# Kernel tuning notes

Hardware: AMD Instinct MI355X
Metric: run time of the kernel (lower is better)

Reference implementation:

```python
import jax, jax.numpy as jnp
import numpy as np
from jax import lax

GLOBAL_BITS = 5
N_LEVELS = float(2 ** GLOBAL_BITS - 1)  # 31


@jax.custom_vjp
def sigmoid_quant(x):
    # round(x * n * 0.4) / n, clamped to [0, 1]
    return jnp.clip(jnp.round(x * (N_LEVELS * 0.4)) / N_LEVELS, 0.0, 1.0)

def _sigq_fwd(x):
    return sigmoid_quant(x), x

def _sigq_bwd(x, g):
    # STE: pass-through, zeroed where |x| >= 2.5 (torch uses ge/le)
    return (jnp.where((x >= 2.5) | (x <= -2.5), 0.0, g),)

sigmoid_quant.defvjp(_sigq_fwd, _sigq_bwd)


@jax.custom_vjp
def tanh_quant(x):
    # round(x * n) / n, clamped to [-1, 1]
    return jnp.clip(jnp.round(x * N_LEVELS) / N_LEVELS, -1.0, 1.0)

def _tanhq_fwd(x):
    return tanh_quant(x), x

def _tanhq_bwd(x, g):
    return (jnp.where((x >= 1.0) | (x <= -1.0), 0.0, g),)

tanh_quant.defvjp(_tanhq_fwd, _tanhq_bwd)


def gru_layer(x, Wh, bh, Wz, bz, Wr, br, Uh, Uz, Ur):
    """x: [T, B, D_in] -> hiddens [T, B, H]. Quantized GRU, test mode (drop=0)."""
    T, B, _ = x.shape
    H = Wh.shape[0]
    # Precompute input projections over all timesteps (as the torch code does).
    wh = jnp.einsum('tbd,hd->tbh', x, Wh) + bh
    wz = jnp.einsum('tbd,hd->tbh', x, Wz) + bz
    wr = jnp.einsum('tbd,hd->tbh', x, Wr) + br

    def step(h, gates):
        whk, wzk, wrk = gates
        zt = sigmoid_quant(wzk + h @ Uz.T)
        rt = sigmoid_quant(wrk + h @ Ur.T)
        at = whk + (rt * h) @ Uh.T
        hcand = tanh_quant(at)  # drop_mask == 1.0 in test mode
        h_new = zt * h + (1.0 - zt) * hcand
        return h_new, h_new

    h0 = jnp.zeros((B, H), dtype=x.dtype)
    _, hs = lax.scan(step, h0, (wh, wz, wr))
    return hs


def _layer_params(key, d_in, h):
    ks = jax.random.split(key, 6)
    s_in = 1.0 / np.sqrt(d_in)
    s_h = 1.0 / np.sqrt(h)
    return dict(
        Wh=jax.random.uniform(ks[0], (h, d_in), jnp.float32, -s_in, s_in),
        bh=jnp.zeros((h,), jnp.float32),
        Wz=jax.random.uniform(ks[1], (h, d_in), jnp.float32, -s_in, s_in),
        bz=jnp.zeros((h,), jnp.float32),
        Wr=jax.random.uniform(ks[2], (h, d_in), jnp.float32, -s_in, s_in),
        br=jnp.zeros((h,), jnp.float32),
        Uh=jax.random.uniform(ks[3], (h, h), jnp.float32, -s_h, s_h),
        Uz=jax.random.uniform(ks[4], (h, h), jnp.float32, -s_h, s_h),
        Ur=jax.random.uniform(ks[5], (h, h), jnp.float32, -s_h, s_h),
    )


def setup_inputs() -> dict:
    T, B, D, H, C = 200, 512, 40, 400, 12
    key = jax.random.key(0)
    kx, k0, k1, kfc = jax.random.split(key, 4)
    inp = {"x": jax.random.normal(kx, (T, B, D), jnp.float32)}
    p0 = _layer_params(k0, D, H)
    p1 = _layer_params(k1, H, H)
    for name, v in p0.items():
        inp[name + "0"] = v
    for name, v in p1.items():
        inp[name + "1"] = v
    s = 1.0 / np.sqrt(H)
    inp["Wfc"] = jax.random.uniform(kfc, (C, H), jnp.float32, -s, s)
    inp["bfc"] = jnp.zeros((C,), jnp.float32)
    return inp


def reference(x, Wh0, bh0, Wz0, bz0, Wr0, br0, Uh0, Uz0, Ur0,
              Wh1, bh1, Wz1, bz1, Wr1, br1, Uh1, Uz1, Ur1, Wfc, bfc):
    h = gru_layer(x, Wh0, bh0, Wz0, bz0, Wr0, br0, Uh0, Uz0, Ur0)
    h = gru_layer(h, Wh1, bh1, Wz1, bz1, Wr1, br1, Uh1, Uz1, Ur1)
    out = h[-1]                 # [B, H] last timestep
    logits = out @ Wfc.T + bfc  # [B, C]
    return jax.nn.softmax(logits, axis=-1)
```

## Files before the change

### kernel.cpp

```cpp
#include <hip/hip_runtime.h>
#include <math.h>

#define TT 200
#define BB 512
#define DD 40
#define HH 400
#define NC 12
#define NBLK 500
#define NTHR 256


struct P {
  const float *x;
  const float *Wh0,*bh0,*Wz0,*bz0,*Wr0,*br0,*Uh0,*Uz0,*Ur0;
  const float *Wh1,*bh1,*Wz1,*bz1,*Wr1,*br1,*Uh1,*Uz1,*Ur1;
  const float *Wfc,*bfc;
  float *h0a,*h0b,*h1a,*h1b;
  float *rt1,*zt1,*ah1p,*rt0n,*zt0n;
  unsigned *bar;
  float *out;
};

__device__ __forceinline__ float sigq(float x){
  float v = rintf(x * 12.4f) / 31.0f;
  return fminf(fmaxf(v, 0.0f), 1.0f);
}
__device__ __forceinline__ float tanhq(float x){
  float v = rintf(x * 31.0f) / 31.0f;
  return fminf(fmaxf(v, -1.0f), 1.0f);
}

__device__ void load_slice(float* dst, const float* __restrict__ Wg, int ldw,
                           int j0, int K, int tid){
  const int c  = tid >> 4;
  const int ks = tid & 15;
  for (int k = ks; k < K; k += 16)
    dst[k*16 + c] = Wg[(size_t)(j0 + c)*ldw + k];
}

__device__ __forceinline__ void gaccL(const float* __restrict__ A, int lda,
                                      const float* __restrict__ Wl,
                                      int r, int cb, int K, float acc[2][4]){
  const float4* a0 = (const float4*)(A + (size_t)r*lda);
  const float4* a1 = (const float4*)(A + (size_t)r*lda + lda);
  const int K4 = K >> 2;
  #pragma unroll 4
  for (int k = 0; k < K4; ++k) {
    float4 av0 = a0[k], av1 = a1[k];
    float a0v[4] = {av0.x, av0.y, av0.z, av0.w};
    float a1v[4] = {av1.x, av1.y, av1.z, av1.w};
    #pragma unroll
    for (int i = 0; i < 4; ++i) {
      float4 wv = *(const float4*)(Wl + (k*4+i)*16 + cb);
      acc[0][0]+=a0v[i]*wv.x; acc[0][1]+=a0v[i]*wv.y; acc[0][2]+=a0v[i]*wv.z; acc[0][3]+=a0v[i]*wv.w;
      acc[1][0]+=a1v[i]*wv.x; acc[1][1]+=a1v[i]*wv.y; acc[1][2]+=a1v[i]*wv.z; acc[1][3]+=a1v[i]*wv.w;
    }
  }
}

__device__ __forceinline__ void paccL(const float* __restrict__ Ap,
                                      const float* __restrict__ Am,
                                      const float* __restrict__ Wl,
                                      int r, int cb, int K, float acc[2][4]){
  const float4* p0 = (const float4*)(Ap + (size_t)r*HH);
  const float4* p1 = (const float4*)(Ap + (size_t)r*HH + HH);
  const float4* m0 = (const float4*)(Am + (size_t)r*HH);
  const float4* m1 = (const float4*)(Am + (size_t)r*HH + HH);
  const int K4 = K >> 2;
  #pragma unroll 4
  for (int k = 0; k < K4; ++k) {
    float4 pv0 = p0[k], mv0 = m0[k], pv1 = p1[k], mv1 = m1[k];
    float a0v[4] = {pv0.x*mv0.x, pv0.y*mv0.y, pv0.z*mv0.z, pv0.w*mv0.w};
    float a1v[4] = {pv1.x*mv1.x, pv1.y*mv1.y, pv1.z*mv1.z, pv1.w*mv1.w};
    #pragma unroll
    for (int i = 0; i < 4; ++i) {
      float4 wv = *(const float4*)(Wl + (k*4+i)*16 + cb);
      acc[0][0]+=a0v[i]*wv.x; acc[0][1]+=a0v[i]*wv.y; acc[0][2]+=a0v[i]*wv.z; acc[0][3]+=a0v[i]*wv.w;
      acc[1][0]+=a1v[i]*wv.x; acc[1][1]+=a1v[i]*wv.y; acc[1][2]+=a1v[i]*wv.z; acc[1][3]+=a1v[i]*wv.w;
    }
  }
}

__device__ __forceinline__ void gaccG(const float* __restrict__ A, int lda,
                                      const float* __restrict__ W, int ldw,
                                      int r, int c0, int K, float acc[2][4]){
  const float4* a0 = (const float4*)(A + (size_t)r*lda);
  const float4* a1 = (const float4*)(A + (size_t)r*lda + lda);
  const int K4 = K >> 2;
  for (int k = 0; k < K4; ++k) {
    float4 av0 = a0[k], av1 = a1[k];
    #pragma unroll
    for (int j = 0; j < 4; ++j) {
      float4 wv = *(const float4*)(W + (size_t)(c0+j)*ldw + k*4);
      acc[0][j]+=av0.x*wv.x; acc[0][j]+=av0.y*wv.y; acc[0][j]+=av0.z*wv.z; acc[0][j]+=av0.w*wv.w;
      acc[1][j]+=av1.x*wv.x; acc[1][j]+=av1.y*wv.y; acc[1][j]+=av1.z*wv.z; acc[1][j]+=av1.w*wv.w;
    }
  }
}

__device__ void beta_wave(const P& p, int t, int bm, int bj0, int r, int cb,
                          const float* Wb0, const float* Wb1){
  const float* h0n = (t & 1) ? p.h0b : p.h0a;
  const float* h1c = (t & 1) ? p.h1b : p.h1a;
  const float* xt1 = p.x + (size_t)((t+1) % TT) * BB * DD;
  float acc[2][4] = {};
  const float* bias; float* out; int act = 1;
  if (bm == 0)      { gaccL(h1c,HH,Wb0,r,cb,HH,acc); gaccL(h0n,HH,Wb1,r,cb,HH,acc); bias=p.br1; out=p.rt1; }
  else if (bm == 1) { gaccL(h1c,HH,Wb0,r,cb,HH,acc); gaccL(h0n,HH,Wb1,r,cb,HH,acc); bias=p.bz1; out=p.zt1; }
  else if (bm == 2) { gaccL(h0n,HH,Wb0,r,cb,HH,acc); bias=p.bh1; out=p.ah1p; act=0; }
  else if (bm == 3) { gaccL(h0n,HH,Wb0,r,cb,HH,acc); gaccL(xt1,DD,Wb1,r,cb,DD,acc); bias=p.br0; out=p.rt0n; }
  else              { gaccL(h0n,HH,Wb0,r,cb,HH,acc); gaccL(xt1,DD,Wb1,r,cb,DD,acc); bias=p.bz0; out=p.zt0n; }
  const int c0 = bj0 + cb;
  #pragma unroll
  for (int i = 0; i < 2; ++i) {
    float4 v;
    v.x = acc[i][0] + bias[c0+0];
    v.y = acc[i][1] + bias[c0+1];
    v.z = acc[i][2] + bias[c0+2];
    v.w = acc[i][3] + bias[c0+3];
    if (act) { v.x = sigq(v.x); v.y = sigq(v.y); v.z = sigq(v.z); v.w = sigq(v.w); }
    *(float4*)(out + (size_t)(r+i)*HH + c0) = v;
  }
}

__device__ void alpha_wave(const P& p, int t, int am, int aj0, int r, int cb,
                           const float* Wa, const float* Wa2){
  const float* h0n = (t & 1) ? p.h0b : p.h0a;
  const float* h1c = (t & 1) ? p.h1b : p.h1a;
  float* h0w = (t & 1) ? p.h0a : p.h0b;
  float* h1w = (t & 1) ? p.h1a : p.h1b;
  const float* xt1 = p.x + (size_t)((t+1) % TT) * BB * DD;
  float acc[2][4] = {};
  const int c0 = aj0 + cb;
  if (am == 0) {
    paccL(p.rt1, h1c, Wa, r, cb, HH, acc);
    #pragma unroll
    for (int i = 0; i < 2; ++i) {
      size_t base = (size_t)(r+i)*HH + c0;
      float4 ap = *(const float4*)(p.ah1p + base);
      float4 z  = *(const float4*)(p.zt1 + base);
      float4 hv = *(const float4*)(h1c + base);
      float4 o;
      o.x = z.x*hv.x + (1.0f - z.x)*tanhq(acc[i][0] + ap.x);
      o.y = z.y*hv.y + (1.0f - z.y)*tanhq(acc[i][1] + ap.y);
      o.z = z.z*hv.z + (1.0f - z.z)*tanhq(acc[i][2] + ap.z);
      o.w = z.w*hv.w + (1.0f - z.w)*tanhq(acc[i][3] + ap.w);
      *(float4*)(h1w + base) = o;
    }
  } else {
    paccL(p.rt0n, h0n, Wa, r, cb, HH, acc);
    gaccL(xt1, DD, Wa2, r, cb, DD, acc);
    #pragma unroll
    for (int i = 0; i < 2; ++i) {
      size_t base = (size_t)(r+i)*HH + c0;
      float4 z  = *(const float4*)(p.zt0n + base);
      float4 hv = *(const float4*)(h0n + base);
      float4 o;
      o.x = z.x*hv.x + (1.0f - z.x)*tanhq(acc[i][0] + p.bh0[c0+0]);
      o.y = z.y*hv.y + (1.0f - z.y)*tanhq(acc[i][1] + p.bh0[c0+1]);
      o.z = z.z*hv.z + (1.0f - z.z)*tanhq(acc[i][2] + p.bh0[c0+2]);
      o.w = z.w*hv.w + (1.0f - z.w)*tanhq(acc[i][3] + p.bh0[c0+3]);
      *(float4*)(h0w + base) = o;
    }
  }
}

__device__ void pro_wave(const P& p, int coltile, int r, int cb){
  const int c0 = coltile*16 + cb;
  float accz[2][4] = {}, acca[2][4] = {};
  gaccG(p.x, DD, p.Wz0, DD, r, c0, DD, accz);
  gaccG(p.x, DD, p.Wh0, DD, r, c0, DD, acca);
  #pragma unroll
  for (int i = 0; i < 2; ++i) {
    float4 o;
    float z;
    z = sigq(accz[i][0] + p.bz0[c0+0]); o.x = (1.0f - z)*tanhq(acca[i][0] + p.bh0[c0+0]);
    z = sigq(accz[i][1] + p.bz0[c0+1]); o.y = (1.0f - z)*tanhq(acca[i][1] + p.bh0[c0+1]);
    z = sigq(accz[i][2] + p.bz0[c0+2]); o.z = (1.0f - z)*tanhq(acca[i][2] + p.bh0[c0+2]);
    z = sigq(accz[i][3] + p.bz0[c0+3]); o.w = (1.0f - z)*tanhq(acca[i][3] + p.bh0[c0+3]);
    *(float4*)(p.h0a + (size_t)(r+i)*HH + c0) = o;
  }
}

__device__ void fc_wave(const P& p, int b, int lane){
  const float* h1 = p.h1a;
  float l[NC];
  #pragma unroll
  for (int cI = 0; cI < NC; ++cI) {
    float sm = 0.0f;
    for (int k = lane; k < HH; k += 64)
      sm += h1[(size_t)b*HH + k] * p.Wfc[(size_t)cI*HH + k];
    #pragma unroll
    for (int off = 32; off > 0; off >>= 1)
      sm += __shfl_xor(sm, off);
    l[cI] = sm + p.bfc[cI];
  }
  float mx = l[0];
  #pragma unroll
  for (int cI = 1; cI < NC; ++cI) mx = fmaxf(mx, l[cI]);
  float sum = 0.0f;
  #pragma unroll
  for (int cI = 0; cI < NC; ++cI) { l[cI] = expf(l[cI] - mx); sum += l[cI]; }
  float inv = 1.0f / sum;
  if (lane == 0) {
    #pragma unroll
    for (int cI = 0; cI < NC; ++cI) p.out[(size_t)b*NC + cI] = l[cI] * inv;
  }
}

__device__ void gbar(int bn, unsigned* bar, int u){
  __syncthreads();
  if (threadIdx.x == 0) {
    __threadfence();
    const int i = u & 15;
    const int quota = (NBLK >> 4) + ((i < (NBLK & 15)) ? 1 : 0);
    unsigned* c0  = bar + i*32;
    unsigned* c1  = bar + 512;
    unsigned* gen = bar + 544;
    unsigned v = __hip_atomic_fetch_add(c0, 1u, __ATOMIC_RELEASE, __HIP_MEMORY_SCOPE_AGENT);
    if (v + 1u == (unsigned)quota * (unsigned)(bn+1)) {
      unsigned w2 = __hip_atomic_fetch_add(c1, 1u, __ATOMIC_ACQ_REL, __HIP_MEMORY_SCOPE_AGENT);
      if (w2 + 1u == 16u * (unsigned)(bn+1))
        __hip_atomic_store(gen, (unsigned)(bn+1), __ATOMIC_RELEASE, __HIP_MEMORY_SCOPE_AGENT);
    }
    while (__hip_atomic_load(gen, __ATOMIC_RELAXED, __HIP_MEMORY_SCOPE_AGENT) < (unsigned)(bn+1))
      __builtin_amdgcn_s_sleep(2);
    __threadfence();
  }
  __syncthreads();
}

__device__ void load_beta_lds(const P& p, int bm, int bj0, float* Wb0, float* Wb1, int tid){
  if (bm == 0)      { load_slice(Wb0, p.Ur1, HH, bj0, HH, tid); load_slice(Wb1, p.Wr1, HH, bj0, HH, tid); }
  else if (bm == 1) { load_slice(Wb0, p.Uz1, HH, bj0, HH, tid); load_slice(Wb1, p.Wz1, HH, bj0, HH, tid); }
  else if (bm == 2) { load_slice(Wb0, p.Wh1, HH, bj0, HH, tid); }
  else if (bm == 3) { load_slice(Wb0, p.Ur0, HH, bj0, HH, tid); load_slice(Wb1, p.Wr0, DD, bj0, DD, tid); }
  else              { load_slice(Wb0, p.Uz0, HH, bj0, HH, tid); load_slice(Wb1, p.Wz0, DD, bj0, DD, tid); }
}
__device__ void load_alpha_lds(const P& p, int am, int aj0, float* Wa, float* Wa2, int tid){
  if (am == 0) load_slice(Wa, p.Uh1, HH, aj0, HH, tid);
  else       { load_slice(Wa, p.Uh0, HH, aj0, HH, tid); load_slice(Wa2, p.Wh0, DD, aj0, DD, tid); }
}

__global__ __launch_bounds__(NTHR, 2) void gru_coop(P p){
  __shared__ float lds[19840];
  float* Wb0 = lds;
  float* Wb1 = lds + 6400;
  float* Wa  = lds + 12800;
  float* Wa2 = lds + 19200;

  const int u    = blockIdx.x;
  const int tid  = threadIdx.x;
  const int w    = tid >> 6;
  const int lane = tid & 63;

  const int bkey = u >> 2, bq = u & 3;
  const int bm = bkey / 25, bj0 = (bkey % 25) * 16;
  const int akey = u >> 2;
  const int am = akey / 25, aj0 = (akey % 25) * 16;

  const int r  = bq*128 + w*32 + (lane & 15)*2;
  const int cb = (lane >> 4) * 4;

  load_beta_lds(p, bm, bj0, Wb0, Wb1, tid);
  if (u < 200) load_alpha_lds(p, am, aj0, Wa, Wa2, tid);
  if (u < 100) pro_wave(p, u >> 2, (u & 3)*128 + w*32 + (lane & 15)*2, cb);

  int bn = 0;
  gbar(bn++, p.bar, u);
  for (int t = 0; t < TT; ++t) {
    beta_wave(p, t, bm, bj0, r, cb, Wb0, Wb1);
    gbar(bn++, p.bar, u);
    if (u < 200) alpha_wave(p, t, am, aj0, r, cb, Wa, Wa2);
    gbar(bn++, p.bar, u);
  }
  if (u < 128) fc_wave(p, u*4 + w, lane);
}

__global__ __launch_bounds__(NTHR) void k_pro(P p){
  const int u = blockIdx.x, tid = threadIdx.x, w = tid >> 6, lane = tid & 63;
  pro_wave(p, u >> 2, (u & 3)*128 + w*32 + (lane & 15)*2, ((lane >> 4)*4));
}
__global__ __launch_bounds__(NTHR) void k_beta(P p, int t){
  __shared__ float lds[12800];
  const int u = blockIdx.x, tid = threadIdx.x, w = tid >> 6, lane = tid & 63;
  const int bkey = u >> 2, bq = u & 3;
  const int bm = bkey / 25, bj0 = (bkey % 25) * 16;
  load_beta_lds(p, bm, bj0, lds, lds + 6400, tid);
  __syncthreads();
  beta_wave(p, t, bm, bj0, bq*128 + w*32 + (lane & 15)*2, (lane >> 4)*4, lds, lds + 6400);
}
__global__ __launch_bounds__(NTHR) void k_alpha(P p, int t){
  __shared__ float lds[7040];
  const int u = blockIdx.x, tid = threadIdx.x, w = tid >> 6, lane = tid & 63;
  const int akey = u >> 2, aq = u & 3;
  const int am = akey / 25, aj0 = (akey % 25) * 16;
  load_alpha_lds(p, am, aj0, lds, lds + 6400, tid);
  __syncthreads();
  alpha_wave(p, t, am, aj0, aq*128 + w*32 + (lane & 15)*2, (lane >> 4)*4, lds, lds + 6400);
}
__global__ __launch_bounds__(NTHR) void k_fc(P p){
  const int w = threadIdx.x >> 6, lane = threadIdx.x & 63;
  fc_wave(p, blockIdx.x*4 + w, lane);
}

extern "C" void kernel_launch(void* const* d_in, const int* in_sizes, int n_in,
                              void* d_out, int out_size, void* d_ws, size_t ws_size,
                              hipStream_t stream) {
  P p;
  p.x   = (const float*)d_in[0];
  p.Wh0 = (const float*)d_in[1];  p.bh0 = (const float*)d_in[2];
  p.Wz0 = (const float*)d_in[3];  p.bz0 = (const float*)d_in[4];
  p.Wr0 = (const float*)d_in[5];  p.br0 = (const float*)d_in[6];
  p.Uh0 = (const float*)d_in[7];  p.Uz0 = (const float*)d_in[8];  p.Ur0 = (const float*)d_in[9];
  p.Wh1 = (const float*)d_in[10]; p.bh1 = (const float*)d_in[11];
  p.Wz1 = (const float*)d_in[12]; p.bz1 = (const float*)d_in[13];
  p.Wr1 = (const float*)d_in[14]; p.br1 = (const float*)d_in[15];
  p.Uh1 = (const float*)d_in[16]; p.Uz1 = (const float*)d_in[17]; p.Ur1 = (const float*)d_in[18];
  p.Wfc = (const float*)d_in[19]; p.bfc = (const float*)d_in[20];

  float* ws = (float*)d_ws;
  const size_t SZ = (size_t)BB * HH;
  p.h0a  = ws + 0*SZ;  p.h0b  = ws + 1*SZ;
  p.h1a  = ws + 2*SZ;  p.h1b  = ws + 3*SZ;
  p.rt1  = ws + 4*SZ;  p.zt1  = ws + 5*SZ;  p.ah1p = ws + 6*SZ;
  p.rt0n = ws + 7*SZ;  p.zt0n = ws + 8*SZ;
  p.bar  = (unsigned*)(ws + 9*SZ);
  p.out  = (float*)d_out;

  hipMemsetAsync(p.h1a, 0, SZ*sizeof(float), stream);
  hipMemsetAsync(p.bar, 0, 4096, stream);

  void* args[] = { &p };
  hipError_t err = hipLaunchCooperativeKernel((const void*)gru_coop, dim3(NBLK),
                                              dim3(NTHR), args, 0, stream);
  if (err != hipSuccess) {
    k_pro<<<dim3(100), dim3(NTHR), 0, stream>>>(p);
    for (int t = 0; t < TT; ++t) {
      k_beta <<<dim3(NBLK), dim3(NTHR), 0, stream>>>(p, t);
      k_alpha<<<dim3(200),  dim3(NTHR), 0, stream>>>(p, t);
    }
    k_fc<<<dim3(128), dim3(NTHR), 0, stream>>>(p);
  }
}
```

Baseline: 33.75 ms.

## Transpose hidden-state layout to column-major and give each thread 16 output columns

Hidden state and gate buffers now use a [H][B] layout. Each thread owns one batch row and computes 16 output columns, so the LDS weight reads become broadcasts and the activation loads are coalesced. The grid is halved to 250 blocks. The input x is transposed into double-buffered xta/xtb scratch by idle blocks during the alpha phase. The cost is one batch element per thread with scalar strided loads and 16 accumulators per thread, which means fewer, fatter waves.

```diff
diff --git a/kernel.cpp b/kernel.cpp
--- a/kernel.cpp
+++ b/kernel.cpp
@@ -6,7 +6,7 @@
 #define DD 40
 #define HH 400
 #define NC 12
-#define NBLK 500
+#define NBLK 250
 #define NTHR 256
 
 
@@ -17,6 +17,7 @@
   const float *Wfc,*bfc;
   float *h0a,*h0b,*h1a,*h1b;
   float *rt1,*zt1,*ah1p,*rt0n,*zt0n;
+  float *xta,*xtb;
   unsigned *bar;
   float *out;
 };
@@ -32,153 +33,133 @@
 
 __device__ void load_slice(float* dst, const float* __restrict__ Wg, int ldw,
                            int j0, int K, int tid){
-  const int c  = tid >> 4;
-  const int ks = tid & 15;
-  for (int k = ks; k < K; k += 16)
+  const int c  = tid & 15;
+  const int kb = tid >> 4;
+  for (int k = kb; k < K; k += 16)
     dst[k*16 + c] = Wg[(size_t)(j0 + c)*ldw + k];
 }
 
-__device__ __forceinline__ void gaccL(const float* __restrict__ A, int lda,
+__device__ __forceinline__ void gaccT(const float* __restrict__ A,
                                       const float* __restrict__ Wl,
-                                      int r, int cb, int K, float acc[2][4]){
-  const float4* a0 = (const float4*)(A + (size_t)r*lda);
-  const float4* a1 = (const float4*)(A + (size_t)r*lda + lda);
+                                      int b, int K, float acc[16]){
+  const float* ap = A + b;
   const int K4 = K >> 2;
-  #pragma unroll 4
-  for (int k = 0; k < K4; ++k) {
-    float4 av0 = a0[k], av1 = a1[k];
-    float a0v[4] = {av0.x, av0.y, av0.z, av0.w};
-    float a1v[4] = {av1.x, av1.y, av1.z, av1.w};
-    #pragma unroll
-    for (int i = 0; i < 4; ++i) {
-      float4 wv = *(const float4*)(Wl + (k*4+i)*16 + cb);
-      acc[0][0]+=a0v[i]*wv.x; acc[0][1]+=a0v[i]*wv.y; acc[0][2]+=a0v[i]*wv.z; acc[0][3]+=a0v[i]*wv.w;
-      acc[1][0]+=a1v[i]*wv.x; acc[1][1]+=a1v[i]*wv.y; acc[1][2]+=a1v[i]*wv.z; acc[1][3]+=a1v[i]*wv.w;
-    }
-  }
-}
-
-__device__ __forceinline__ void paccL(const float* __restrict__ Ap,
+  #pragma unroll 2
+  for (int g = 0; g < K4; ++g) {
+    float a[4];
+    #pragma unroll
+    for (int kk = 0; kk < 4; ++kk) a[kk] = ap[(size_t)(g*4+kk)*BB];
+    #pragma unroll
+    for (int kk = 0; kk < 4; ++kk) {
+      const float4* w = (const float4*)(Wl + (g*4+kk)*16);
+      float4 w0 = w[0], w1 = w[1], w2 = w[2], w3 = w[3];
+      float av = a[kk];
+      acc[0] +=av*w0.x; acc[1] +=av*w0.y; acc[2] +=av*w0.z; acc[3] +=av*w0.w;
+      acc[4] +=av*w1.x; acc[5] +=av*w1.y; acc[6] +=av*w1.z; acc[7] +=av*w1.w;
+      acc[8] +=av*w2.x; acc[9] +=av*w2.y; acc[10]+=av*w2.z; acc[11]+=av*w2.w;
+      acc[12]+=av*w3.x; acc[13]+=av*w3.y; acc[14]+=av*w3.z; acc[15]+=av*w3.w;
+    }
+  }
+}
+
+__device__ __forceinline__ void paccT(const float* __restrict__ Ap,
                                       const float* __restrict__ Am,
                                       const float* __restrict__ Wl,
-                                      int r, int cb, int K, float acc[2][4]){
-  const float4* p0 = (const float4*)(Ap + (size_t)r*HH);
-  const float4* p1 = (const float4*)(Ap + (size_t)r*HH + HH);
-  const float4* m0 = (const float4*)(Am + (size_t)r*HH);
-  const float4* m1 = (const float4*)(Am + (size_t)r*HH + HH);
+                                      int b, int K, float acc[16]){
+  const float* pp = Ap + b;
+  const float* mp = Am + b;
   const int K4 = K >> 2;
-  #pragma unroll 4
-  for (int k = 0; k < K4; ++k) {
-    float4 pv0 = p0[k], mv0 = m0[k], pv1 = p1[k], mv1 = m1[k];
-    float a0v[4] = {pv0.x*mv0.x, pv0.y*mv0.y, pv0.z*mv0.z, pv0.w*mv0.w};
-    float a1v[4] = {pv1.x*mv1.x, pv1.y*mv1.y, pv1.z*mv1.z, pv1.w*mv1.w};
-    #pragma unroll
-    for (int i = 0; i < 4; ++i) {
-      float4 wv = *(const float4*)(Wl + (k*4+i)*16 + cb);
-      acc[0][0]+=a0v[i]*wv.x; acc[0][1]+=a0v[i]*wv.y; acc[0][2]+=a0v[i]*wv.z; acc[0][3]+=a0v[i]*wv.w;
-      acc[1][0]+=a1v[i]*wv.x; acc[1][1]+=a1v[i]*wv.y; acc[1][2]+=a1v[i]*wv.z; acc[1][3]+=a1v[i]*wv.w;
-    }
-  }
-}
-
-__device__ __forceinline__ void gaccG(const float* __restrict__ A, int lda,
-                                      const float* __restrict__ W, int ldw,
-                                      int r, int c0, int K, float acc[2][4]){
-  const float4* a0 = (const float4*)(A + (size_t)r*lda);
-  const float4* a1 = (const float4*)(A + (size_t)r*lda + lda);
-  const int K4 = K >> 2;
-  for (int k = 0; k < K4; ++k) {
-    float4 av0 = a0[k], av1 = a1[k];
-    #pragma unroll
-    for (int j = 0; j < 4; ++j) {
-      float4 wv = *(const float4*)(W + (size_t)(c0+j)*ldw + k*4);
-      acc[0][j]+=av0.x*wv.x; acc[0][j]+=av0.y*wv.y; acc[0][j]+=av0.z*wv.z; acc[0][j]+=av0.w*wv.w;
-      acc[1][j]+=av1.x*wv.x; acc[1][j]+=av1.y*wv.y; acc[1][j]+=av1.z*wv.z; acc[1][j]+=av1.w*wv.w;
-    }
-  }
-}
-
-__device__ void beta_wave(const P& p, int t, int bm, int bj0, int r, int cb,
+  #pragma unroll 2
+  for (int g = 0; g < K4; ++g) {
+    float a[4];
+    #pragma unroll
+    for (int kk = 0; kk < 4; ++kk)
+      a[kk] = pp[(size_t)(g*4+kk)*BB] * mp[(size_t)(g*4+kk)*BB];
+    #pragma unroll
+    for (int kk = 0; kk < 4; ++kk) {
+      const float4* w = (const float4*)(Wl + (g*4+kk)*16);
+      float4 w0 = w[0], w1 = w[1], w2 = w[2], w3 = w[3];
+      float av = a[kk];
+      acc[0] +=av*w0.x; acc[1] +=av*w0.y; acc[2] +=av*w0.z; acc[3] +=av*w0.w;
+      acc[4] +=av*w1.x; acc[5] +=av*w1.y; acc[6] +=av*w1.z; acc[7] +=av*w1.w;
+      acc[8] +=av*w2.x; acc[9] +=av*w2.y; acc[10]+=av*w2.z; acc[11]+=av*w2.w;
+      acc[12]+=av*w3.x; acc[13]+=av*w3.y; acc[14]+=av*w3.z; acc[15]+=av*w3.w;
+    }
+  }
+}
+
+__device__ void xpose(const float* __restrict__ xsrc, float* dst, int d, int tid){
+  for (int b = tid; b < BB; b += NTHR)
+    dst[d*BB + b] = xsrc[(size_t)b*DD + d];
+}
+
+__device__ void beta_wave(const P& p, int t, int bm, int c0, int b,
                           const float* Wb0, const float* Wb1){
   const float* h0n = (t & 1) ? p.h0b : p.h0a;
   const float* h1c = (t & 1) ? p.h1b : p.h1a;
-  const float* xt1 = p.x + (size_t)((t+1) % TT) * BB * DD;
-  float acc[2][4] = {};
+  const float* xt1 = (t & 1) ? p.xta : p.xtb;
+
+  float acc[16] = {};
   const float* bias; float* out; int act = 1;
-  if (bm == 0)      { gaccL(h1c,HH,Wb0,r,cb,HH,acc); gaccL(h0n,HH,Wb1,r,cb,HH,acc); bias=p.br1; out=p.rt1; }
-  else if (bm == 1) { gaccL(h1c,HH,Wb0,r,cb,HH,acc); gaccL(h0n,HH,Wb1,r,cb,HH,acc); bias=p.bz1; out=p.zt1; }
-  else if (bm == 2) { gaccL(h0n,HH,Wb0,r,cb,HH,acc); bias=p.bh1; out=p.ah1p; act=0; }
-  else if (bm == 3) { gaccL(h0n,HH,Wb0,r,cb,HH,acc); gaccL(xt1,DD,Wb1,r,cb,DD,acc); bias=p.br0; out=p.rt0n; }
-  else              { gaccL(h0n,HH,Wb0,r,cb,HH,acc); gaccL(xt1,DD,Wb1,r,cb,DD,acc); bias=p.bz0; out=p.zt0n; }
-  const int c0 = bj0 + cb;
-  #pragma unroll
-  for (int i = 0; i < 2; ++i) {
-    float4 v;
-    v.x = acc[i][0] + bias[c0+0];
-    v.y = acc[i][1] + bias[c0+1];
-    v.z = acc[i][2] + bias[c0+2];
-    v.w = acc[i][3] + bias[c0+3];
-    if (act) { v.x = sigq(v.x); v.y = sigq(v.y); v.z = sigq(v.z); v.w = sigq(v.w); }
-    *(float4*)(out + (size_t)(r+i)*HH + c0) = v;
-  }
-}
-
-__device__ void alpha_wave(const P& p, int t, int am, int aj0, int r, int cb,
+  if (bm == 0)      { gaccT(h1c,Wb0,b,HH,acc); gaccT(h0n,Wb1,b,HH,acc); bias=p.br1; out=p.rt1; }
+  else if (bm == 1) { gaccT(h1c,Wb0,b,HH,acc); gaccT(h0n,Wb1,b,HH,acc); bias=p.bz1; out=p.zt1; }
+  else if (bm == 2) { gaccT(h0n,Wb0,b,HH,acc); bias=p.bh1; out=p.ah1p; act=0; }
+  else if (bm == 3) { gaccT(h0n,Wb0,b,HH,acc); gaccT(xt1,Wb1,b,DD,acc); bias=p.br0; out=p.rt0n; }
+  else              { gaccT(h0n,Wb0,b,HH,acc); gaccT(xt1,Wb1,b,DD,acc); bias=p.bz0; out=p.zt0n; }
+
+  #pragma unroll
+  for (int c = 0; c < 16; ++c) {
+    float v = acc[c] + bias[c0+c];
+    out[(size_t)(c0+c)*BB + b] = act ? sigq(v) : v;
+  }
+}
+
+__device__ void alpha_wave(const P& p, int t, int am, int c0, int b,
                            const float* Wa, const float* Wa2){
   const float* h0n = (t & 1) ? p.h0b : p.h0a;
   const float* h1c = (t & 1) ? p.h1b : p.h1a;
   float* h0w = (t & 1) ? p.h0a : p.h0b;
   float* h1w = (t & 1) ? p.h1a : p.h1b;
-  const float* xt1 = p.x + (size_t)((t+1) % TT) * BB * DD;
-  float acc[2][4] = {};
-  const int c0 = aj0 + cb;
+  const float* xt1 = (t & 1) ? p.xta : p.xtb;
+
+  float acc[16] = {};
   if (am == 0) {
-    paccL(p.rt1, h1c, Wa, r, cb, HH, acc);
-    #pragma unroll
-    for (int i = 0; i < 2; ++i) {
-      size_t base = (size_t)(r+i)*HH + c0;
-      float4 ap = *(const float4*)(p.ah1p + base);
-      float4 z  = *(const float4*)(p.zt1 + base);
-      float4 hv = *(const float4*)(h1c + base);
-      float4 o;
-      o.x = z.x*hv.x + (1.0f - z.x)*tanhq(acc[i][0] + ap.x);
-      o.y = z.y*hv.y + (1.0f - z.y)*tanhq(acc[i][1] + ap.y);
-      o.z = z.z*hv.z + (1.0f - z.z)*tanhq(acc[i][2] + ap.z);
-      o.w = z.w*hv.w + (1.0f - z.w)*tanhq(acc[i][3] + ap.w);
-      *(float4*)(h1w + base) = o;
+    paccT(p.rt1, h1c, Wa, b, HH, acc);
+    #pragma unroll
+    for (int c = 0; c < 16; ++c) {
+      size_t idx = (size_t)(c0+c)*BB + b;
+      float at = acc[c] + p.ah1p[idx];
+      float z = p.zt1[idx], hv = h1c[idx];
+      h1w[idx] = z*hv + (1.0f - z)*tanhq(at);
     }
   } else {
-    paccL(p.rt0n, h0n, Wa, r, cb, HH, acc);
-    gaccL(xt1, DD, Wa2, r, cb, DD, acc);
-    #pragma unroll
-    for (int i = 0; i < 2; ++i) {
-      size_t base = (size_t)(r+i)*HH + c0;
-      float4 z  = *(const float4*)(p.zt0n + base);
-      float4 hv = *(const float4*)(h0n + base);
-      float4 o;
-      o.x = z.x*hv.x + (1.0f - z.x)*tanhq(acc[i][0] + p.bh0[c0+0]);
-      o.y = z.y*hv.y + (1.0f - z.y)*tanhq(acc[i][1] + p.bh0[c0+1]);
-      o.z = z.z*hv.z + (1.0f - z.z)*tanhq(acc[i][2] + p.bh0[c0+2]);
-      o.w = z.w*hv.w + (1.0f - z.w)*tanhq(acc[i][3] + p.bh0[c0+3]);
-      *(float4*)(h0w + base) = o;
-    }
-  }
-}
-
-__device__ void pro_wave(const P& p, int coltile, int r, int cb){
-  const int c0 = coltile*16 + cb;
-  float accz[2][4] = {}, acca[2][4] = {};
-  gaccG(p.x, DD, p.Wz0, DD, r, c0, DD, accz);
-  gaccG(p.x, DD, p.Wh0, DD, r, c0, DD, acca);
-  #pragma unroll
-  for (int i = 0; i < 2; ++i) {
-    float4 o;
-    float z;
-    z = sigq(accz[i][0] + p.bz0[c0+0]); o.x = (1.0f - z)*tanhq(acca[i][0] + p.bh0[c0+0]);
-    z = sigq(accz[i][1] + p.bz0[c0+1]); o.y = (1.0f - z)*tanhq(acca[i][1] + p.bh0[c0+1]);
-    z = sigq(accz[i][2] + p.bz0[c0+2]); o.z = (1.0f - z)*tanhq(acca[i][2] + p.bh0[c0+2]);
-    z = sigq(accz[i][3] + p.bz0[c0+3]); o.w = (1.0f - z)*tanhq(acca[i][3] + p.bh0[c0+3]);
-    *(float4*)(p.h0a + (size_t)(r+i)*HH + c0) = o;
+    paccT(p.rt0n, h0n, Wa, b, HH, acc);
+    gaccT(xt1, Wa2, b, DD, acc);
+    #pragma unroll
+    for (int c = 0; c < 16; ++c) {
+      size_t idx = (size_t)(c0+c)*BB + b;
+      float at = acc[c] + p.bh0[c0+c];
+      float z = p.zt0n[idx], hv = h0n[idx];
+      h0w[idx] = z*hv + (1.0f - z)*tanhq(at);
+    }
+  }
+}
+
+__device__ void pro_wave(const P& p, int c0, int b){
+  float az[16] = {}, ah[16] = {};
+  for (int d = 0; d < DD; ++d) {
+    float av = p.xta[d*BB + b];
+    #pragma unroll
+    for (int c = 0; c < 16; ++c) {
+      az[c] += av * p.Wz0[(size_t)(c0+c)*DD + d];
+      ah[c] += av * p.Wh0[(size_t)(c0+c)*DD + d];
+    }
+  }
+  #pragma unroll
+  for (int c = 0; c < 16; ++c) {
+    float z = sigq(az[c] + p.bz0[c0+c]);
+    float a = ah[c] + p.bh0[c0+c];
+    p.h0a[(size_t)(c0+c)*BB + b] = (1.0f - z)*tanhq(a);
   }
 }
 
@@ -189,7 +170,7 @@
   for (int cI = 0; cI < NC; ++cI) {
     float sm = 0.0f;
     for (int k = lane; k < HH; k += 64)
-      sm += h1[(size_t)b*HH + k] * p.Wfc[(size_t)cI*HH + k];
+      sm += h1[(size_t)k*BB + b] * p.Wfc[(size_t)cI*HH + k];
     #pragma unroll
     for (int off = 32; off > 0; off >>= 1)
       sm += __shfl_xor(sm, off);
@@ -230,16 +211,16 @@
   __syncthreads();
 }
 
-__device__ void load_beta_lds(const P& p, int bm, int bj0, float* Wb0, float* Wb1, int tid){
-  if (bm == 0)      { load_slice(Wb0, p.Ur1, HH, bj0, HH, tid); load_slice(Wb1, p.Wr1, HH, bj0, HH, tid); }
-  else if (bm == 1) { load_slice(Wb0, p.Uz1, HH, bj0, HH, tid); load_slice(Wb1, p.Wz1, HH, bj0, HH, tid); }
-  else if (bm == 2) { load_slice(Wb0, p.Wh1, HH, bj0, HH, tid); }
-  else if (bm == 3) { load_slice(Wb0, p.Ur0, HH, bj0, HH, tid); load_slice(Wb1, p.Wr0, DD, bj0, DD, tid); }
-  else              { load_slice(Wb0, p.Uz0, HH, bj0, HH, tid); load_slice(Wb1, p.Wz0, DD, bj0, DD, tid); }
-}
-__device__ void load_alpha_lds(const P& p, int am, int aj0, float* Wa, float* Wa2, int tid){
-  if (am == 0) load_slice(Wa, p.Uh1, HH, aj0, HH, tid);
-  else       { load_slice(Wa, p.Uh0, HH, aj0, HH, tid); load_slice(Wa2, p.Wh0, DD, aj0, DD, tid); }
+__device__ void load_beta_lds(const P& p, int bm, int j0, float* Wb0, float* Wb1, int tid){
+  if (bm == 0)      { load_slice(Wb0, p.Ur1, HH, j0, HH, tid); load_slice(Wb1, p.Wr1, HH, j0, HH, tid); }
+  else if (bm == 1) { load_slice(Wb0, p.Uz1, HH, j0, HH, tid); load_slice(Wb1, p.Wz1, HH, j0, HH, tid); }
+  else if (bm == 2) { load_slice(Wb0, p.Wh1, HH, j0, HH, tid); }
+  else if (bm == 3) { load_slice(Wb0, p.Ur0, HH, j0, HH, tid); load_slice(Wb1, p.Wr0, DD, j0, DD, tid); }
+  else              { load_slice(Wb0, p.Uz0, HH, j0, HH, tid); load_slice(Wb1, p.Wz0, DD, j0, DD, tid); }
+}
+__device__ void load_alpha_lds(const P& p, int am, int j0, float* Wa, float* Wa2, int tid){
+  if (am == 0) load_slice(Wa, p.Uh1, HH, j0, HH, tid);
+  else       { load_slice(Wa, p.Uh0, HH, j0, HH, tid); load_slice(Wa2, p.Wh0, DD, j0, DD, tid); }
 }
 
 __global__ __launch_bounds__(NTHR, 2) void gru_coop(P p){
@@ -249,59 +230,65 @@
   float* Wa  = lds + 12800;
   float* Wa2 = lds + 19200;
 
-  const int u    = blockIdx.x;
-  const int tid  = threadIdx.x;
-  const int w    = tid >> 6;
-  const int lane = tid & 63;
-
-  const int bkey = u >> 2, bq = u & 3;
-  const int bm = bkey / 25, bj0 = (bkey % 25) * 16;
-  const int akey = u >> 2;
-  const int am = akey / 25, aj0 = (akey % 25) * 16;
-
-  const int r  = bq*128 + w*32 + (lane & 15)*2;
-  const int cb = (lane >> 4) * 4;
-
-  load_beta_lds(p, bm, bj0, Wb0, Wb1, tid);
-  if (u < 200) load_alpha_lds(p, am, aj0, Wa, Wa2, tid);
-  if (u < 100) pro_wave(p, u >> 2, (u & 3)*128 + w*32 + (lane & 15)*2, cb);
-
+  const int u   = blockIdx.x;
+  const int tid = threadIdx.x;
+  const int bk  = u >> 1;
+  const int bm  = bk / 25, bc0 = (bk % 25) * 16;
+  const int am  = bk / 25, ac0 = bc0;
+  const int b   = (u & 1)*256 + tid;
+
+  load_beta_lds(p, bm, bc0, Wb0, Wb1, tid);
+  if (u < 100) load_alpha_lds(p, am, ac0, Wa, Wa2, tid);
+
+  if (u < 40)       xpose(p.x,                       p.xta, u,      tid);
+  else if (u < 80)  xpose(p.x + (size_t)BB*DD,       p.xtb, u - 40, tid);
   int bn = 0;
   gbar(bn++, p.bar, u);
+  if (u < 50) pro_wave(p, (u >> 1)*16, b);
+  gbar(bn++, p.bar, u);
+
   for (int t = 0; t < TT; ++t) {
-    beta_wave(p, t, bm, bj0, r, cb, Wb0, Wb1);
+    beta_wave(p, t, bm, bc0, b, Wb0, Wb1);
     gbar(bn++, p.bar, u);
-    if (u < 200) alpha_wave(p, t, am, aj0, r, cb, Wa, Wa2);
+    if (u < 100) alpha_wave(p, t, am, ac0, b, Wa, Wa2);
+    else if (u < 140)
+      xpose(p.x + (size_t)((t+2) % TT)*BB*DD, (t & 1) ? p.xtb : p.xta, u - 100, tid);
     gbar(bn++, p.bar, u);
   }
-  if (u < 128) fc_wave(p, u*4 + w, lane);
-}
-
+  if (u < 128) fc_wave(p, u*4 + (tid >> 6), tid & 63);
+}
+
+__global__ __launch_bounds__(NTHR) void k_init(P p){
+  const int u = blockIdx.x, tid = threadIdx.x;
+  if (u < 40)      xpose(p.x,                 p.xta, u,      tid);
+  else if (u < 80) xpose(p.x + (size_t)BB*DD, p.xtb, u - 40, tid);
+}
 __global__ __launch_bounds__(NTHR) void k_pro(P p){
-  const int u = blockIdx.x, tid = threadIdx.x, w = tid >> 6, lane = tid & 63;
-  pro_wave(p, u >> 2, (u & 3)*128 + w*32 + (lane & 15)*2, ((lane >> 4)*4));
+  const int u = blockIdx.x;
+  pro_wave(p, (u >> 1)*16, (u & 1)*256 + threadIdx.x);
 }
 __global__ __launch_bounds__(NTHR) void k_beta(P p, int t){
   __shared__ float lds[12800];
-  const int u = blockIdx.x, tid = threadIdx.x, w = tid >> 6, lane = tid & 63;
-  const int bkey = u >> 2, bq = u & 3;
-  const int bm = bkey / 25, bj0 = (bkey % 25) * 16;
-  load_beta_lds(p, bm, bj0, lds, lds + 6400, tid);
+  const int u = blockIdx.x, tid = threadIdx.x;
+  const int bk = u >> 1, bm = bk / 25, bc0 = (bk % 25) * 16;
+  load_beta_lds(p, bm, bc0, lds, lds + 6400, tid);
   __syncthreads();
-  beta_wave(p, t, bm, bj0, bq*128 + w*32 + (lane & 15)*2, (lane >> 4)*4, lds, lds + 6400);
+  beta_wave(p, t, bm, bc0, (u & 1)*256 + tid, lds, lds + 6400);
 }
 __global__ __launch_bounds__(NTHR) void k_alpha(P p, int t){
   __shared__ float lds[7040];
-  const int u = blockIdx.x, tid = threadIdx.x, w = tid >> 6, lane = tid & 63;
-  const int akey = u >> 2, aq = u & 3;
-  const int am = akey / 25, aj0 = (akey % 25) * 16;
-  load_alpha_lds(p, am, aj0, lds, lds + 6400, tid);
-  __syncthreads();
-  alpha_wave(p, t, am, aj0, aq*128 + w*32 + (lane & 15)*2, (lane >> 4)*4, lds, lds + 6400);
+  const int u = blockIdx.x, tid = threadIdx.x;
+  if (u < 100) {
+    const int ak = u >> 1, am = ak / 25, ac0 = (ak % 25) * 16;
+    load_alpha_lds(p, am, ac0, lds, lds + 6400, tid);
+    __syncthreads();
+    alpha_wave(p, t, am, ac0, (u & 1)*256 + tid, lds, lds + 6400);
+  } else if (u < 140) {
+    xpose(p.x + (size_t)((t+2) % TT)*BB*DD, (t & 1) ? p.xtb : p.xta, u - 100, tid);
+  }
 }
 __global__ __launch_bounds__(NTHR) void k_fc(P p){
-  const int w = threadIdx.x >> 6, lane = threadIdx.x & 63;
-  fc_wave(p, blockIdx.x*4 + w, lane);
+  fc_wave(p, blockIdx.x*4 + (threadIdx.x >> 6), threadIdx.x & 63);
 }
 
 extern "C" void kernel_launch(void* const* d_in, const int* in_sizes, int n_in,
@@ -325,7 +312,9 @@
   p.h1a  = ws + 2*SZ;  p.h1b  = ws + 3*SZ;
   p.rt1  = ws + 4*SZ;  p.zt1  = ws + 5*SZ;  p.ah1p = ws + 6*SZ;
   p.rt0n = ws + 7*SZ;  p.zt0n = ws + 8*SZ;
-  p.bar  = (unsigned*)(ws + 9*SZ);
+  p.xta  = ws + 9*SZ;
+  p.xtb  = p.xta + (size_t)BB*DD;
+  p.bar  = (unsigned*)(p.xtb + (size_t)BB*DD);
   p.out  = (float*)d_out;
 
   hipMemsetAsync(p.h1a, 0, SZ*sizeof(float), stream);
@@ -335,10 +324,11 @@
   hipError_t err = hipLaunchCooperativeKernel((const void*)gru_coop, dim3(NBLK),
                                               dim3(NTHR), args, 0, stream);
   if (err != hipSuccess) {
-    k_pro<<<dim3(100), dim3(NTHR), 0, stream>>>(p);
+    k_init<<<dim3(80), dim3(NTHR), 0, stream>>>(p);
+    k_pro<<<dim3(50), dim3(NTHR), 0, stream>>>(p);
     for (int t = 0; t < TT; ++t) {
       k_beta <<<dim3(NBLK), dim3(NTHR), 0, stream>>>(p, t);
-      k_alpha<<<dim3(200),  dim3(NTHR), 0, stream>>>(p, t);
+      k_alpha<<<dim3(140),  dim3(NTHR), 0, stream>>>(p, t);
     }
     k_fc<<<dim3(128), dim3(NTHR), 0, stream>>>(p);
   }
```

After: 41.09 ms. 1.22x slower.
